# Kernel tuning notes

Measured on AMD Instinct MI355X. Metric: run time of the kernel, lower is better.

The kernel has to match this reference:

```python
import jax, jax.numpy as jnp
import numpy as np

N_NODES = 100000
N_EDGES = 1600000
N_GRAPHS = 512
IN_DIM = 128
D = 128
N_CLASSES = 10


def gcn_layer(x, src, dst, W, b, n_nodes):
    """PyG GCNConv: out = D^{-1/2}(A+I)D^{-1/2} (x W) + b, deg over dst col + self-loop."""
    h = x @ W  # [N, d]
    deg = jax.ops.segment_sum(jnp.ones(src.shape[0], x.dtype), dst,
                              num_segments=n_nodes) + 1.0  # self-loop adds 1
    dinv = jax.lax.rsqrt(deg)  # deg >= 1 so always finite
    norm = dinv[src] * dinv[dst]  # [E]
    agg = jax.ops.segment_sum(h[src] * norm[:, None], dst, num_segments=n_nodes)
    agg = agg + h * (dinv * dinv)[:, None]  # self-loop message: dinv_i^2 * h_i
    return agg + b


def setup_inputs() -> dict:
    key = jax.random.key(0)
    ks = jax.random.split(key, 10)
    s = 0.05
    return {
        "x": jax.random.normal(ks[0], (N_NODES, IN_DIM), jnp.float32),
        "c_2": jax.random.randint(ks[1], (N_EDGES,), 0, N_NODES, jnp.int64),
        "u_2": jax.random.randint(ks[2], (N_EDGES,), 0, N_NODES, jnp.int64),
        "batch": jnp.sort(jax.random.randint(ks[3], (N_NODES,), 0, N_GRAPHS, jnp.int64)),
        "W_enc": jax.random.normal(ks[4], (IN_DIM, D), jnp.float32) * s,
        "b_enc": jnp.zeros((D,), jnp.float32),
        "W1": jax.random.normal(ks[5], (D, D), jnp.float32) * s,
        "b1": jnp.zeros((D,), jnp.float32),
        "W2": jax.random.normal(ks[6], (D, D), jnp.float32) * s,
        "b2": jnp.zeros((D,), jnp.float32),
        "W3": jax.random.normal(ks[7], (D, D), jnp.float32) * s,
        "b3": jnp.zeros((D,), jnp.float32),
        "Wr1": jax.random.normal(ks[8], (D, D), jnp.float32) * s,
        "br1": jnp.zeros((D,), jnp.float32),
        "Wr2": jax.random.normal(ks[9], (D, N_CLASSES), jnp.float32) * s,
        "br2": jnp.zeros((N_CLASSES,), jnp.float32),
    }


def reference(x, c_2, u_2, batch, W_enc, b_enc, W1, b1, W2, b2, W3, b3,
              Wr1, br1, Wr2, br2):
    h = x @ W_enc + b_enc
    for W, b in ((W1, b1), (W2, b2), (W3, b3)):
        h = gcn_layer(h, c_2, u_2, W, b, N_NODES)
        h = jax.nn.relu(h)  # dropout is identity in eval mode
    # global_add_pool over graph assignment
    g = jax.ops.segment_sum(h, batch, num_segments=N_GRAPHS)  # [G, d]
    logits = jax.nn.relu(g @ Wr1 + br1) @ Wr2 + br2  # [G, num_classes]
    return logits
```

## Files before the change

kernel.cpp:

```cpp
#include <hip/hip_runtime.h>
#include <hip/hip_bf16.h>

#define NN 100000
#define NE 1600000
#define NG 512
#define NC 10
#define NBINS 196
#define BINCAP 10240
#define EPB 8192

typedef __attribute__((ext_vector_type(8))) short bf16x8;
typedef __attribute__((ext_vector_type(4))) float f32x4;
typedef int int4a __attribute__((ext_vector_type(4), aligned(4)));

__device__ __forceinline__ float bflo(unsigned u) { return __uint_as_float(u << 16); }
__device__ __forceinline__ float bfhi(unsigned u) { return __uint_as_float(u & 0xffff0000u); }
__device__ __forceinline__ unsigned short f2bf(float f) {
  unsigned u = __float_as_uint(f);
  unsigned r = u + 0x7fffu + ((u >> 16) & 1u);
  return (unsigned short)(r >> 16);
}


__global__ __launch_bounds__(256) void k_bininit(int* __restrict__ binCursor) {
  int t = threadIdx.x;
  if (t < NBINS) binCursor[t] = t * BINCAP;
}

__global__ __launch_bounds__(256) void k_binp1(const int* __restrict__ src, const int* __restrict__ dst,
                                               int* __restrict__ binCursor, unsigned* __restrict__ stage) {
  __shared__ unsigned srec[EPB];
  __shared__ unsigned char sbin[EPB];
  __shared__ int cnt[NBINS], pre[NBINS], base[NBINS], lcur[NBINS];
  __shared__ int tmp[256];
  int t = threadIdx.x;
  if (t < NBINS) { cnt[t] = 0; lcur[t] = 0; }
  __syncthreads();
  int e0 = blockIdx.x * EPB;
  unsigned myrec[32];
  short mybin[32];
#pragma unroll
  for (int i = 0; i < 32; ++i) {
    int e = e0 + i * 256 + t;
    if (e < NE) {
      int s = src[e], d = dst[e];
      int b = d >> 9;
      mybin[i] = (short)b;
      myrec[i] = ((unsigned)s << 9) | (unsigned)(d & 511);
      atomicAdd(&cnt[b], 1);
    } else mybin[i] = -1;
  }
  __syncthreads();
  int c0 = (t < NBINS) ? cnt[t] : 0;
  tmp[t] = c0;
  __syncthreads();
  for (int o = 1; o < 256; o <<= 1) { int v = (t >= o) ? tmp[t - o] : 0; __syncthreads(); tmp[t] += v; __syncthreads(); }
  if (t < NBINS) pre[t] = tmp[t] - c0;
  __syncthreads();
  if (t < NBINS && c0 > 0) base[t] = atomicAdd(&binCursor[t], c0);
  __syncthreads();
#pragma unroll
  for (int i = 0; i < 32; ++i) {
    int b = mybin[i];
    if (b >= 0) {
      int r = atomicAdd(&lcur[b], 1);
      int pos = pre[b] + r;
      srec[pos] = myrec[i];
      sbin[pos] = (unsigned char)b;
    }
  }
  __syncthreads();
  int total = NE - e0; if (total > EPB) total = EPB;
  for (int sidx = t; sidx < total; sidx += 256) {
    int b = sbin[sidx];
    stage[base[b] + (sidx - pre[b])] = srec[sidx];
  }
}

__global__ __launch_bounds__(256) void k_binp2(const unsigned* __restrict__ stage, const int* __restrict__ binCursor,
                                               int* __restrict__ csr_src, int* __restrict__ offs,
                                               int* __restrict__ deg, float* __restrict__ dinv) {
  __shared__ int ldeg[512], loff[512], lcur[512];
  __shared__ int sbc[NBINS], sbb[NBINS];
  __shared__ int tmp[256];
  __shared__ unsigned sorted[BINCAP];
  int b = blockIdx.x, t = threadIdx.x;
  int n0 = b << 9;
  int sbase = b * BINCAP;
  int cnt = binCursor[b] - sbase; if (cnt > BINCAP) cnt = BINCAP;
  for (int i = t; i < 512; i += 256) { ldeg[i] = 0; lcur[i] = 0; }
  if (t < NBINS) sbc[t] = 0;
  __syncthreads();
  for (int j = t; j < cnt; j += 256) {
    unsigned r = stage[sbase + j];
    atomicAdd(&ldeg[r & 511], 1);
    atomicAdd(&sbc[r >> 18], 1);
  }
  __syncthreads();
  int i2 = t * 2;
  int a0 = ldeg[i2], a1 = ldeg[i2 + 1];
  int s = a0 + a1;
  tmp[t] = s;
  __syncthreads();
  for (int o = 1; o < 256; o <<= 1) { int v = (t >= o) ? tmp[t - o] : 0; __syncthreads(); tmp[t] += v; __syncthreads(); }
  int ex = tmp[t] - s;
  loff[i2] = ex;
  loff[i2 + 1] = ex + a0;
  int nd0 = n0 + i2, nd1 = n0 + i2 + 1;
  if (nd0 < NN) { offs[nd0] = sbase + ex;      deg[nd0] = a0; dinv[nd0] = rsqrtf((float)a0 + 1.0f); }
  if (nd1 < NN) { offs[nd1] = sbase + ex + a0; deg[nd1] = a1; dinv[nd1] = rsqrtf((float)a1 + 1.0f); }
  __syncthreads();
  int c0 = (t < NBINS) ? sbc[t] : 0;
  tmp[t] = c0;
  __syncthreads();
  for (int o = 1; o < 256; o <<= 1) { int v = (t >= o) ? tmp[t - o] : 0; __syncthreads(); tmp[t] += v; __syncthreads(); }
  if (t < NBINS) { sbb[t] = tmp[t] - c0; sbc[t] = 0; }
  __syncthreads();
  for (int j = t; j < cnt; j += 256) {
    unsigned r = stage[sbase + j];
    int bk = r >> 18;
    sorted[sbb[bk] + atomicAdd(&sbc[bk], 1)] = r;
  }
  __syncthreads();
  for (int j = t; j < cnt; j += 256) {
    unsigned r = sorted[j];
    int li = r & 511;
    int pos = atomicAdd(&lcur[li], 1);
    csr_src[sbase + loff[li] + pos] = (int)(r >> 9);
  }
}

__global__ __launch_bounds__(256) void k_wt4(const float* __restrict__ Wa, const float* __restrict__ Wb,
                                             const float* __restrict__ Wc, const float* __restrict__ Wd,
                                             unsigned short* __restrict__ Ta, unsigned short* __restrict__ Tb,
                                             unsigned short* __restrict__ Tc, unsigned short* __restrict__ Td) {
  int w = blockIdx.x >> 6;
  const float* W = (w == 0) ? Wa : (w == 1) ? Wb : (w == 2) ? Wc : Wd;
  unsigned short* T = (w == 0) ? Ta : (w == 1) ? Tb : (w == 2) ? Tc : Td;
  int idx = (blockIdx.x & 63) * 256 + threadIdx.x;
  int k = idx >> 7, c = idx & 127;
  T[c * 128 + k] = f2bf(W[k * 128 + c]);
}


template<int ADD_BIAS, int RELU, int SRC_F32, int SCALE_ROW>
__global__ __launch_bounds__(256) void k_gemm_mfma(const void* __restrict__ Ap,
                                                   const unsigned short* __restrict__ Wt,
                                                   const float* __restrict__ bias,
                                                   const float* __restrict__ dinv,
                                                   unsigned short* __restrict__ Out, int M) {
  __shared__ uint4 Al4[2048];
  __shared__ uint4 Wl4[2048];
  int row0 = blockIdx.x * 128;
  const uint4* W16 = (const uint4*)Wt;
#pragma unroll
  for (int it = 0; it < 8; ++it) {
    int idx = it * 256 + threadIdx.x;
    int r = idx >> 4, c = idx & 15;
    int gr = row0 + r;
    uint4 v = make_uint4(0, 0, 0, 0);
    if (gr < M) {
      if (SRC_F32) {
        const float4* Af = (const float4*)Ap;
        float4 f0 = Af[(size_t)gr * 32 + c * 2];
        float4 f1 = Af[(size_t)gr * 32 + c * 2 + 1];
        v.x = (unsigned)f2bf(f0.x) | ((unsigned)f2bf(f0.y) << 16);
        v.y = (unsigned)f2bf(f0.z) | ((unsigned)f2bf(f0.w) << 16);
        v.z = (unsigned)f2bf(f1.x) | ((unsigned)f2bf(f1.y) << 16);
        v.w = (unsigned)f2bf(f1.z) | ((unsigned)f2bf(f1.w) << 16);
      } else {
        v = ((const uint4*)Ap)[(size_t)gr * 16 + c];
      }
    }
    Al4[r * 16 + (c ^ (r & 15))] = v;
    Wl4[r * 16 + (c ^ (r & 15))] = W16[idx];
  }
  __syncthreads();

  int lane = threadIdx.x & 63;
  int wid = threadIdx.x >> 6;
  int wr = wid >> 1, wc = wid & 1;
  int lr = lane & 15, kb = lane >> 4;

  f32x4 acc[4][4] = {};
#pragma unroll
  for (int ks = 0; ks < 4; ++ks) {
    int c = ks * 4 + kb;
    bf16x8 af[4], bfr[4];
#pragma unroll
    for (int i = 0; i < 4; ++i) {
      int ar = wr * 64 + i * 16 + lr;
      af[i] = *(const bf16x8*)&Al4[ar * 16 + (c ^ lr)];
      int bc = wc * 64 + i * 16 + lr;
      bfr[i] = *(const bf16x8*)&Wl4[bc * 16 + (c ^ lr)];
    }
#pragma unroll
    for (int i = 0; i < 4; ++i)
#pragma unroll
      for (int n = 0; n < 4; ++n)
        acc[i][n] = __builtin_amdgcn_mfma_f32_16x16x32_bf16(af[i], bfr[n], acc[i][n], 0, 0, 0);
  }

  float bcol[4];
  if (ADD_BIAS) {
#pragma unroll
    for (int n = 0; n < 4; ++n) bcol[n] = bias[wc * 64 + n * 16 + lr];
  }
#pragma unroll
  for (int i = 0; i < 4; ++i) {
    int rbase = row0 + wr * 64 + i * 16 + kb * 4;
#pragma unroll
    for (int n = 0; n < 4; ++n) {
      int col = wc * 64 + n * 16 + lr;
#pragma unroll
      for (int j = 0; j < 4; ++j) {
        int gr = rbase + j;
        if (gr < M) {
          float v = acc[i][n][j];
          if (ADD_BIAS) v += bcol[n];
          if (RELU) v = fmaxf(v, 0.f);
          if (SCALE_ROW) v *= dinv[gr];
          Out[(size_t)gr * 128 + col] = f2bf(v);
        }
      }
    }
  }
}


__global__ __launch_bounds__(256) void k_agg(const unsigned short* __restrict__ hs,
                                             const int* __restrict__ offs, const int* __restrict__ deg,
                                             const float* __restrict__ dinv,
                                             const int* __restrict__ csr_src,
                                             const float* __restrict__ bias,
                                             unsigned short* __restrict__ out) {
  int node = blockIdx.x * 4 + (threadIdx.x >> 6);
  if (node >= NN) return;
  int l = threadIdx.x & 63;
  const unsigned* hs32 = (const unsigned*)hs;
  float di = dinv[node];
  unsigned v = hs32[(size_t)node * 64 + l];
  float ax = bflo(v), ay = bfhi(v);
  int p0 = offs[node], n = deg[node];
  int p = 0;
  for (; p + 16 <= n; p += 16) {
    const int* cp = csr_src + p0 + p;
    int4a i0 = *(const int4a*)cp;
    int4a i1 = *(const int4a*)(cp + 4);
    int4a i2 = *(const int4a*)(cp + 8);
    int4a i3 = *(const int4a*)(cp + 12);
    unsigned u0  = hs32[(size_t)i0.x * 64 + l], u1  = hs32[(size_t)i0.y * 64 + l];
    unsigned u2  = hs32[(size_t)i0.z * 64 + l], u3  = hs32[(size_t)i0.w * 64 + l];
    unsigned u4  = hs32[(size_t)i1.x * 64 + l], u5  = hs32[(size_t)i1.y * 64 + l];
    unsigned u6  = hs32[(size_t)i1.z * 64 + l], u7  = hs32[(size_t)i1.w * 64 + l];
    unsigned u8  = hs32[(size_t)i2.x * 64 + l], u9  = hs32[(size_t)i2.y * 64 + l];
    unsigned u10 = hs32[(size_t)i2.z * 64 + l], u11 = hs32[(size_t)i2.w * 64 + l];
    unsigned u12 = hs32[(size_t)i3.x * 64 + l], u13 = hs32[(size_t)i3.y * 64 + l];
    unsigned u14 = hs32[(size_t)i3.z * 64 + l], u15 = hs32[(size_t)i3.w * 64 + l];
    ax += bflo(u0) + bflo(u1) + bflo(u2) + bflo(u3) + bflo(u4) + bflo(u5) + bflo(u6) + bflo(u7)
        + bflo(u8) + bflo(u9) + bflo(u10) + bflo(u11) + bflo(u12) + bflo(u13) + bflo(u14) + bflo(u15);
    ay += bfhi(u0) + bfhi(u1) + bfhi(u2) + bfhi(u3) + bfhi(u4) + bfhi(u5) + bfhi(u6) + bfhi(u7)
        + bfhi(u8) + bfhi(u9) + bfhi(u10) + bfhi(u11) + bfhi(u12) + bfhi(u13) + bfhi(u14) + bfhi(u15);
  }
  for (; p + 8 <= n; p += 8) {
    const int* cp = csr_src + p0 + p;
    int4a i0 = *(const int4a*)cp;
    int4a i1 = *(const int4a*)(cp + 4);
    unsigned u0 = hs32[(size_t)i0.x * 64 + l], u1 = hs32[(size_t)i0.y * 64 + l];
    unsigned u2 = hs32[(size_t)i0.z * 64 + l], u3 = hs32[(size_t)i0.w * 64 + l];
    unsigned u4 = hs32[(size_t)i1.x * 64 + l], u5 = hs32[(size_t)i1.y * 64 + l];
    unsigned u6 = hs32[(size_t)i1.z * 64 + l], u7 = hs32[(size_t)i1.w * 64 + l];
    ax += bflo(u0) + bflo(u1) + bflo(u2) + bflo(u3) + bflo(u4) + bflo(u5) + bflo(u6) + bflo(u7);
    ay += bfhi(u0) + bfhi(u1) + bfhi(u2) + bfhi(u3) + bfhi(u4) + bfhi(u5) + bfhi(u6) + bfhi(u7);
  }
  for (; p < n; ++p) {
    int s0 = csr_src[p0 + p];
    unsigned u0 = hs32[(size_t)s0 * 64 + l];
    ax += bflo(u0);
    ay += bfhi(u0);
  }
  float2 b2 = ((const float2*)bias)[l];
  ax = fmaxf(fmaf(ax, di, b2.x), 0.f);
  ay = fmaxf(fmaf(ay, di, b2.y), 0.f);
  ((unsigned*)out)[(size_t)node * 64 + l] = (unsigned)f2bf(ax) | ((unsigned)f2bf(ay) << 16);
}


__device__ __forceinline__ int lowerb(const int* a, int n, int key) {
  int lo = 0, hi = n;
  while (lo < hi) {
    int mid = (lo + hi) >> 1;
    if (a[mid] < key) lo = mid + 1; else hi = mid;
  }
  return lo;
}

__global__ __launch_bounds__(256) void k_pool(const unsigned short* __restrict__ h, const int* __restrict__ batch,
                                              float* __restrict__ g) {
  __shared__ float sx[4][64];
  __shared__ float sy[4][64];
  int gi = blockIdx.x;
  int col = threadIdx.x & 63;
  int rp = threadIdx.x >> 6;
  int lo = lowerb(batch, NN, gi), hi = lowerb(batch, NN, gi + 1);
  const unsigned* h32 = (const unsigned*)h;
  float ax = 0.f, ay = 0.f;
  for (int i = lo + rp; i < hi; i += 4) {
    unsigned u = h32[(size_t)i * 64 + col];
    ax += bflo(u);
    ay += bfhi(u);
  }
  sx[rp][col] = ax;
  sy[rp][col] = ay;
  __syncthreads();
  if (rp == 0) {
    ax = sx[0][col] + sx[1][col] + sx[2][col] + sx[3][col];
    ay = sy[0][col] + sy[1][col] + sy[2][col] + sy[3][col];
    ((float2*)g)[gi * 64 + col] = make_float2(ax, ay);
  }
}

__global__ __launch_bounds__(256) void k_gemm_f32(const float* __restrict__ A, const float* __restrict__ W,
                                                  const float* __restrict__ bias, float* __restrict__ Out,
                                                  int M) {
  __shared__ float4 Wl[128 * 32];
  __shared__ float4 Xl[128 * 32];
  const float4* W4 = (const float4*)W;
  for (int i = threadIdx.x; i < 4096; i += 256) Wl[i] = W4[i];
  int row0 = blockIdx.x * 128;
  const float4* A4 = (const float4*)A;
  for (int i = threadIdx.x; i < 4096; i += 256) {
    int r = i >> 5, g = i & 31;
    int gr = row0 + r;
    float4 v = make_float4(0.f, 0.f, 0.f, 0.f);
    if (gr < M) v = A4[gr * 32 + g];
    Xl[r * 32 + (g ^ ((r >> 3) & 7))] = v;
  }
  __syncthreads();

  int cg = threadIdx.x & 15;
  int rg = threadIdx.x >> 4;
  int swz = rg & 7;
  float acc[8][8] = {};
  for (int g = 0; g < 32; ++g) {
    float4 xv[8];
#pragma unroll
    for (int i = 0; i < 8; ++i) xv[i] = Xl[(rg * 8 + i) * 32 + (g ^ swz)];
#pragma unroll
    for (int kk = 0; kk < 4; ++kk) {
      float4 wa = Wl[(g * 4 + kk) * 32 + cg * 2];
      float4 wb = Wl[(g * 4 + kk) * 32 + cg * 2 + 1];
#pragma unroll
      for (int i = 0; i < 8; ++i) {
        float x = (kk == 0) ? xv[i].x : (kk == 1) ? xv[i].y : (kk == 2) ? xv[i].z : xv[i].w;
        acc[i][0] = fmaf(x, wa.x, acc[i][0]);
        acc[i][1] = fmaf(x, wa.y, acc[i][1]);
        acc[i][2] = fmaf(x, wa.z, acc[i][2]);
        acc[i][3] = fmaf(x, wa.w, acc[i][3]);
        acc[i][4] = fmaf(x, wb.x, acc[i][4]);
        acc[i][5] = fmaf(x, wb.y, acc[i][5]);
        acc[i][6] = fmaf(x, wb.z, acc[i][6]);
        acc[i][7] = fmaf(x, wb.w, acc[i][7]);
      }
    }
  }
  float4 ba = ((const float4*)bias)[cg * 2];
  float4 bb = ((const float4*)bias)[cg * 2 + 1];
#pragma unroll
  for (int i = 0; i < 8; ++i) {
    int gr = row0 + rg * 8 + i;
    if (gr < M) {
      float4 oa, ob;
      oa.x = fmaxf(acc[i][0] + ba.x, 0.f); oa.y = fmaxf(acc[i][1] + ba.y, 0.f);
      oa.z = fmaxf(acc[i][2] + ba.z, 0.f); oa.w = fmaxf(acc[i][3] + ba.w, 0.f);
      ob.x = fmaxf(acc[i][4] + bb.x, 0.f); ob.y = fmaxf(acc[i][5] + bb.y, 0.f);
      ob.z = fmaxf(acc[i][6] + bb.z, 0.f); ob.w = fmaxf(acc[i][7] + bb.w, 0.f);
      ((float4*)Out)[gr * 32 + cg * 2] = oa;
      ((float4*)Out)[gr * 32 + cg * 2 + 1] = ob;
    }
  }
}

__global__ __launch_bounds__(128) void k_cls(const float* __restrict__ t, const float* __restrict__ Wr2,
                                             const float* __restrict__ br2, float* __restrict__ out) {
  int gi = blockIdx.x;
  __shared__ float row[128];
  row[threadIdx.x] = t[gi * 128 + threadIdx.x];
  __syncthreads();
  if (threadIdx.x < NC) {
    float acc = br2[threadIdx.x];
    for (int k = 0; k < 128; ++k) acc = fmaf(row[k], Wr2[k * NC + threadIdx.x], acc);
    out[gi * NC + threadIdx.x] = acc;
  }
}


extern "C" void kernel_launch(void* const* d_in, const int* in_sizes, int n_in,
                              void* d_out, int out_size, void* d_ws, size_t ws_size,
                              hipStream_t stream) {
  const float* x     = (const float*)d_in[0];
  const int*   src   = (const int*)d_in[1];
  const int*   dst   = (const int*)d_in[2];
  const int*   batch = (const int*)d_in[3];
  const float* W_enc = (const float*)d_in[4];
  const float* b_enc = (const float*)d_in[5];
  const float* W1 = (const float*)d_in[6],  *b1 = (const float*)d_in[7];
  const float* W2 = (const float*)d_in[8],  *b2 = (const float*)d_in[9];
  const float* W3 = (const float*)d_in[10], *b3 = (const float*)d_in[11];
  const float* Wr1 = (const float*)d_in[12], *br1 = (const float*)d_in[13];
  const float* Wr2 = (const float*)d_in[14], *br2 = (const float*)d_in[15];
  float* out = (float*)d_out;

  char* ws = (char*)d_ws;
  size_t off = 0;
  auto alloc = [&](size_t bytes) {
    void* p = ws + off;
    off = (off + bytes + 255) & ~(size_t)255;
    return p;
  };
  unsigned short* h   = (unsigned short*)alloc((size_t)NN * 128 * 2);
  unsigned short* hs  = (unsigned short*)alloc((size_t)NN * 128 * 2);
  unsigned short* WtE = (unsigned short*)alloc(128 * 128 * 2);
  unsigned short* Wt1 = (unsigned short*)alloc(128 * 128 * 2);
  unsigned short* Wt2 = (unsigned short*)alloc(128 * 128 * 2);
  unsigned short* Wt3 = (unsigned short*)alloc(128 * 128 * 2);
  int*   deg      = (int*)alloc((size_t)NN * 4);
  float* dinv     = (float*)alloc((size_t)NN * 4);
  int*   offs     = (int*)alloc((size_t)NN * 4);
  int*   binCursor= (int*)alloc(NBINS * 4);
  int*   csr_src  = (int*)alloc((size_t)NBINS * BINCAP * 4);
  unsigned* stage = (unsigned*)alloc((size_t)NBINS * BINCAP * 4);
  float* g        = (float*)alloc((size_t)NG * 128 * 4);
  float* t1       = (float*)alloc((size_t)NG * 128 * 4);

  k_bininit<<<1, 256, 0, stream>>>(binCursor);
  k_binp1<<<(NE + EPB - 1) / EPB, 256, 0, stream>>>(src, dst, binCursor, stage);
  k_binp2<<<NBINS, 256, 0, stream>>>(stage, binCursor, csr_src, offs, deg, dinv);

  k_wt4<<<256, 256, 0, stream>>>(W_enc, W1, W2, W3, WtE, Wt1, Wt2, Wt3);

  int gM = (NN + 127) / 128;
  k_gemm_mfma<1, 0, 1, 0><<<gM, 256, 0, stream>>>(x, WtE, b_enc, nullptr, h, NN);

  const unsigned short* Wts[3] = {Wt1, Wt2, Wt3};
  const float* bs[3] = {b1, b2, b3};
  int gA = (NN + 3) / 4;
  for (int L = 0; L < 3; ++L) {
    k_gemm_mfma<0, 0, 0, 1><<<gM, 256, 0, stream>>>(h, Wts[L], nullptr, dinv, hs, NN);
    k_agg<<<gA, 256, 0, stream>>>(hs, offs, deg, dinv, csr_src, bs[L], h);
  }

  k_pool<<<NG, 256, 0, stream>>>(h, batch, g);
  k_gemm_f32<<<(NG + 127) / 128, 256, 0, stream>>>(g, Wr1, br1, t1, NG);
  k_cls<<<NG, 128, 0, stream>>>(t1, Wr2, br2, out);
}
```

Measured before the change: 437.9 us.

## Fold bin init into weight transpose, drop bucket sort, read weights from global

Merges the bin-cursor initialisation into the weight-transpose kernel as an extra block, removing one launch. Removes the pre-sort by source bucket in the CSR build, so CSR neighbour order is no longer sorted by source range. In the GEMM, the weight tile is read directly from global memory instead of being staged in LDS, halving shared memory per block. The risks are less locality in the aggregation gathers, possibly nondeterministic neighbour order, and uncoalesced global weight loads in the MFMA loop.

```diff
diff --git a/kernel.cpp b/kernel.cpp
--- a/kernel.cpp
+++ b/kernel.cpp
@@ -21,11 +21,6 @@
   return (unsigned short)(r >> 16);
 }
 
-
-__global__ __launch_bounds__(256) void k_bininit(int* __restrict__ binCursor) {
-  int t = threadIdx.x;
-  if (t < NBINS) binCursor[t] = t * BINCAP;
-}
 
 __global__ __launch_bounds__(256) void k_binp1(const int* __restrict__ src, const int* __restrict__ dst,
                                                int* __restrict__ binCursor, unsigned* __restrict__ stage) {
@@ -81,20 +76,16 @@
                                                int* __restrict__ csr_src, int* __restrict__ offs,
                                                int* __restrict__ deg, float* __restrict__ dinv) {
   __shared__ int ldeg[512], loff[512], lcur[512];
-  __shared__ int sbc[NBINS], sbb[NBINS];
   __shared__ int tmp[256];
-  __shared__ unsigned sorted[BINCAP];
   int b = blockIdx.x, t = threadIdx.x;
   int n0 = b << 9;
   int sbase = b * BINCAP;
   int cnt = binCursor[b] - sbase; if (cnt > BINCAP) cnt = BINCAP;
   for (int i = t; i < 512; i += 256) { ldeg[i] = 0; lcur[i] = 0; }
-  if (t < NBINS) sbc[t] = 0;
   __syncthreads();
   for (int j = t; j < cnt; j += 256) {
     unsigned r = stage[sbase + j];
     atomicAdd(&ldeg[r & 511], 1);
-    atomicAdd(&sbc[r >> 18], 1);
   }
   __syncthreads();
   int i2 = t * 2;
@@ -110,30 +101,24 @@
   if (nd0 < NN) { offs[nd0] = sbase + ex;      deg[nd0] = a0; dinv[nd0] = rsqrtf((float)a0 + 1.0f); }
   if (nd1 < NN) { offs[nd1] = sbase + ex + a0; deg[nd1] = a1; dinv[nd1] = rsqrtf((float)a1 + 1.0f); }
   __syncthreads();
-  int c0 = (t < NBINS) ? sbc[t] : 0;
-  tmp[t] = c0;
-  __syncthreads();
-  for (int o = 1; o < 256; o <<= 1) { int v = (t >= o) ? tmp[t - o] : 0; __syncthreads(); tmp[t] += v; __syncthreads(); }
-  if (t < NBINS) { sbb[t] = tmp[t] - c0; sbc[t] = 0; }
-  __syncthreads();
   for (int j = t; j < cnt; j += 256) {
     unsigned r = stage[sbase + j];
-    int bk = r >> 18;
-    sorted[sbb[bk] + atomicAdd(&sbc[bk], 1)] = r;
-  }
-  __syncthreads();
-  for (int j = t; j < cnt; j += 256) {
-    unsigned r = sorted[j];
     int li = r & 511;
     int pos = atomicAdd(&lcur[li], 1);
     csr_src[sbase + loff[li] + pos] = (int)(r >> 9);
   }
 }
 
-__global__ __launch_bounds__(256) void k_wt4(const float* __restrict__ Wa, const float* __restrict__ Wb,
-                                             const float* __restrict__ Wc, const float* __restrict__ Wd,
-                                             unsigned short* __restrict__ Ta, unsigned short* __restrict__ Tb,
-                                             unsigned short* __restrict__ Tc, unsigned short* __restrict__ Td) {
+__global__ __launch_bounds__(256) void k_wt4i(const float* __restrict__ Wa, const float* __restrict__ Wb,
+                                              const float* __restrict__ Wc, const float* __restrict__ Wd,
+                                              unsigned short* __restrict__ Ta, unsigned short* __restrict__ Tb,
+                                              unsigned short* __restrict__ Tc, unsigned short* __restrict__ Td,
+                                              int* __restrict__ binCursor) {
+  if (blockIdx.x == 256) {
+    int t = threadIdx.x;
+    if (t < NBINS) binCursor[t] = t * BINCAP;
+    return;
+  }
   int w = blockIdx.x >> 6;
   const float* W = (w == 0) ? Wa : (w == 1) ? Wb : (w == 2) ? Wc : Wd;
   unsigned short* T = (w == 0) ? Ta : (w == 1) ? Tb : (w == 2) ? Tc : Td;
@@ -150,9 +135,7 @@
                                                    const float* __restrict__ dinv,
                                                    unsigned short* __restrict__ Out, int M) {
   __shared__ uint4 Al4[2048];
-  __shared__ uint4 Wl4[2048];
   int row0 = blockIdx.x * 128;
-  const uint4* W16 = (const uint4*)Wt;
 #pragma unroll
   for (int it = 0; it < 8; ++it) {
     int idx = it * 256 + threadIdx.x;
@@ -173,7 +156,6 @@
       }
     }
     Al4[r * 16 + (c ^ (r & 15))] = v;
-    Wl4[r * 16 + (c ^ (r & 15))] = W16[idx];
   }
   __syncthreads();
 
@@ -181,6 +163,7 @@
   int wid = threadIdx.x >> 6;
   int wr = wid >> 1, wc = wid & 1;
   int lr = lane & 15, kb = lane >> 4;
+  const uint4* W16 = (const uint4*)Wt;
 
   f32x4 acc[4][4] = {};
 #pragma unroll
@@ -192,7 +175,7 @@
       int ar = wr * 64 + i * 16 + lr;
       af[i] = *(const bf16x8*)&Al4[ar * 16 + (c ^ lr)];
       int bc = wc * 64 + i * 16 + lr;
-      bfr[i] = *(const bf16x8*)&Wl4[bc * 16 + (c ^ lr)];
+      bfr[i] = *(const bf16x8*)&W16[bc * 16 + c];
     }
 #pragma unroll
     for (int i = 0; i < 4; ++i)
@@ -433,11 +416,9 @@
   float* g        = (float*)alloc((size_t)NG * 128 * 4);
   float* t1       = (float*)alloc((size_t)NG * 128 * 4);
 
-  k_bininit<<<1, 256, 0, stream>>>(binCursor);
+  k_wt4i<<<257, 256, 0, stream>>>(W_enc, W1, W2, W3, WtE, Wt1, Wt2, Wt3, binCursor);
   k_binp1<<<(NE + EPB - 1) / EPB, 256, 0, stream>>>(src, dst, binCursor, stage);
   k_binp2<<<NBINS, 256, 0, stream>>>(stage, binCursor, csr_src, offs, deg, dinv);
-
-  k_wt4<<<256, 256, 0, stream>>>(W_enc, W1, W2, W3, WtE, Wt1, Wt2, Wt3);
 
   int gM = (NN + 127) / 128;
   k_gemm_mfma<1, 0, 1, 0><<<gM, 256, 0, stream>>>(x, WtE, b_enc, nullptr, h, NN);
```

Result: slower. 448.9 us (+2.5%).
